# Kernel tuning notes

Hardware: AMD Instinct MI355X
Metric: run time of the kernel (lower is better)

The kernel has to match this reference:

```python
import jax, jax.numpy as jnp
import numpy as np

NOPE = 128          # qk_nope_head_dim
ROPE = 64           # qk_rope_head_dim
KV_LORA = 512       # kv_lora_rank
SCALE = (KV_LORA + ROPE) ** (-0.5)


def setup_inputs() -> dict:
    key = jax.random.key(0)
    k1, k2, k3, k4, k5 = jax.random.split(key, 5)
    T, H, K, S = 512, 128, 512, 8192
    q = jax.random.normal(k1, (T, H, NOPE + ROPE), dtype=jnp.float32)
    kv_cache = jax.random.normal(k2, (S, KV_LORA + ROPE), dtype=jnp.float32)
    topk_indices = jax.random.randint(k3, (T, K), 0, S, dtype=jnp.int32)
    k_b_proj_trans = jax.random.normal(k4, (H, KV_LORA, NOPE), dtype=jnp.float32) * 0.02
    v_b_proj = jax.random.normal(k5, (H, 128, KV_LORA), dtype=jnp.float32) * 0.02
    return {"q": q, "kv_cache": kv_cache, "topk_indices": topk_indices,
            "k_b_proj_trans": k_b_proj_trans, "v_b_proj": v_b_proj}


def reference(q, kv_cache, topk_indices, k_b_proj_trans, v_b_proj):
    # q: [T, H, 192]; kv_cache: [S, 576]; topk_indices: [T, K]
    q_nope, q_rope = q[..., :NOPE], q[..., NOPE:]
    # bmm_out(q_nope_t, k_b_proj_trans.transpose(1,2)): [T,H,128] x [H,512,128] -> [T,H,512]
    q_lat = jnp.einsum('thd,hkd->thk', q_nope, k_b_proj_trans)
    q_concat = jnp.concatenate([q_lat, q_rope], axis=-1)        # [T, H, 576]
    # sparse MLA: gather selected latent KV per token
    kv_sel = kv_cache[topk_indices]                              # [T, K, 576]
    scores = jnp.einsum('thc,tkc->thk', q_concat, kv_sel) * SCALE
    p = jax.nn.softmax(scores, axis=-1)                          # [T, H, K]
    attn_lat = jnp.einsum('thk,tkc->thc', p, kv_sel[..., :KV_LORA])  # [T, H, 512]
    # bmm_out(attn_lat_t, v_b_proj.transpose(1,2)): [T,H,512] x [H,512,128] -> [T,H,128]
    out = jnp.einsum('thc,hvc->thv', attn_lat, v_b_proj)
    return out
```

## Files before the change

### kernel.cpp

```cpp
#include <hip/hip_runtime.h>
#include <stdint.h>


#define SCALE 0.041666666666666664f

typedef __bf16 bf16x8 __attribute__((ext_vector_type(8)));
typedef float floatx4 __attribute__((ext_vector_type(4)));
typedef unsigned int uint32x2 __attribute__((ext_vector_type(2)));
typedef unsigned int uint32x4 __attribute__((ext_vector_type(4)));

static __device__ __forceinline__ unsigned short f2bf(float f) {
  unsigned int u = __builtin_bit_cast(unsigned int, f);
  u += 0x7FFF + ((u >> 16) & 1);
  return (unsigned short)(u >> 16);
}
static __device__ __forceinline__ float bf2f(unsigned short h) {
  unsigned int u = ((unsigned int)h) << 16;
  return __builtin_bit_cast(float, u);
}
static __device__ __forceinline__ unsigned int pack2(float lo, float hi) {
  return (unsigned int)f2bf(lo) | ((unsigned int)f2bf(hi) << 16);
}
static __device__ __forceinline__ void ldsdma16(const void* g, void* l) {
  __builtin_amdgcn_global_load_lds(
      (const __attribute__((address_space(1))) void*)g,
      (__attribute__((address_space(3))) void*)l, 16, 0, 0);
}
static __device__ __forceinline__ unsigned int lds_addr(const void* p) {
  return (unsigned int)(unsigned long long)(
      (__attribute__((address_space(3))) const void*)p);
}
#define TR64(dst, addr, OFF) \
  asm volatile("ds_read_b64_tr_b16 %0, %1 offset:" OFF : "=v"(dst) : "v"(addr))

static __device__ __forceinline__ void stage8_f32(const float* __restrict__ src,
                                                  unsigned short* dst) {
  const float4* s4 = reinterpret_cast<const float4*>(src);
  float4 v0 = s4[0], v1 = s4[1];
  uint4 o;
  o.x = pack2(v0.x, v0.y); o.y = pack2(v0.z, v0.w);
  o.z = pack2(v1.x, v1.y); o.w = pack2(v1.z, v1.w);
  *reinterpret_cast<uint4*>(dst) = o;
}

static __device__ __forceinline__ void mfma_4x4(const unsigned short* As,
                                                const unsigned short* Bs,
                                                int wm, int wn, int l15, int quad,
                                                floatx4 acc[4][4]) {
  bf16x8 af[4], bfr[4];
#pragma unroll
  for (int i = 0; i < 4; ++i)
    af[i] = *reinterpret_cast<const bf16x8*>(&As[(wm + i * 16 + l15) * 32 + quad * 8]);
#pragma unroll
  for (int j = 0; j < 4; ++j)
    bfr[j] = *reinterpret_cast<const bf16x8*>(&Bs[(wn + j * 16 + l15) * 32 + quad * 8]);
#pragma unroll
  for (int i = 0; i < 4; ++i)
#pragma unroll
    for (int j = 0; j < 4; ++j)
      acc[i][j] = __builtin_amdgcn_mfma_f32_16x16x32_bf16(af[i], bfr[j], acc[i][j], 0, 0, 0);
}

__global__ void prep(const float* __restrict__ kv, unsigned short* __restrict__ kvb,
                     const float* __restrict__ q, unsigned short* __restrict__ qc) {
  int b = blockIdx.x;
  if (b < 4608) {
    int i = b * 256 + threadIdx.x;
    float4 v = reinterpret_cast<const float4*>(kv)[i];
    ushort4 o;
    o.x = f2bf(v.x); o.y = f2bf(v.y); o.z = f2bf(v.z); o.w = f2bf(v.w);
    reinterpret_cast<ushort4*>(kvb)[i] = o;
  } else {
    int i = (b - 4608) * 256 + threadIdx.x;
    int r = i & 63;
    int th = i >> 6;
    qc[(size_t)th * 576 + 512 + r] = f2bf(q[(size_t)th * 192 + 128 + r] * SCALE);
  }
}

__global__ __launch_bounds__(256) void qlat_gemm(const float* __restrict__ q,
                                                 const float* __restrict__ kb,
                                                 unsigned short* __restrict__ qc) {
  const int h = blockIdx.x;
  const int tm = (blockIdx.y & 3) * 128;
  const int tn = (blockIdx.y >> 2) * 128;
  __shared__ __align__(16) unsigned short As[128 * 32];
  __shared__ __align__(16) unsigned short Bs[128 * 32];
  const int tid = threadIdx.x;
  const int lane = tid & 63, wave = tid >> 6;
  const int wm = (wave & 1) * 64, wn = (wave >> 1) * 64;
  const int l15 = lane & 15, quad = lane >> 4;
  const int r0 = tid >> 2, cg = tid & 3;
  const float* a0 = q + ((size_t)(tm + r0) * 128 + h) * 192 + cg * 8;
  const float* a1 = q + ((size_t)(tm + r0 + 64) * 128 + h) * 192 + cg * 8;
  const float* b0 = kb + ((size_t)h * 512 + tn + r0) * 128 + cg * 8;
  const float* b1 = b0 + (size_t)64 * 128;
  floatx4 acc[4][4] = {};
  for (int ks = 0; ks < 4; ++ks) {
    stage8_f32(a0 + ks * 32, &As[tid * 8]);
    stage8_f32(a1 + ks * 32, &As[2048 + tid * 8]);
    stage8_f32(b0 + ks * 32, &Bs[tid * 8]);
    stage8_f32(b1 + ks * 32, &Bs[2048 + tid * 8]);
    __syncthreads();
    mfma_4x4(As, Bs, wm, wn, l15, quad, acc);
    __syncthreads();
  }
#pragma unroll
  for (int i = 0; i < 4; ++i) {
    const int row = wm + i * 16 + quad * 4;
#pragma unroll
    for (int j = 0; j < 4; ++j) {
      const int col = wn + j * 16 + l15;
#pragma unroll
      for (int r = 0; r < 4; ++r) {
        const int t = tm + row + r;
        qc[((size_t)t * 128 + h) * 576 + tn + col] = f2bf(acc[i][j][r] * SCALE);
      }
    }
  }
}

__global__ __launch_bounds__(256) void scores_gemm(const unsigned short* __restrict__ qc,
                                                   const unsigned short* __restrict__ kvb,
                                                   const int* __restrict__ topk,
                                                   unsigned short* __restrict__ P) {
  const int t = blockIdx.x;
  const int tn = blockIdx.y * 128;
  __shared__ __align__(16) unsigned short As[3][128 * 32];
  __shared__ __align__(16) unsigned short Bs[3][128 * 32];
  const int tid = threadIdx.x;
  const int lane = tid & 63, wave = tid >> 6;
  const int wm = (wave & 1) * 64, wn = (wave >> 1) * 64;
  const int l15 = lane & 15, quad = lane >> 4;
  const int r0 = tid >> 2, cg = tid & 3;
  const unsigned short* a0 = qc + ((size_t)t * 128 + r0) * 576 + cg * 8;
  const unsigned short* a1 = a0 + (size_t)64 * 576;
  const int idx0 = topk[t * 512 + tn + r0];
  const int idx1 = topk[t * 512 + tn + r0 + 64];
  const unsigned short* b0 = kvb + (size_t)idx0 * 576 + cg * 8;
  const unsigned short* b1 = kvb + (size_t)idx1 * 576 + cg * 8;
  floatx4 acc[4][4] = {};
#pragma unroll
  for (int p = 0; p < 2; ++p) {
    ldsdma16(a0 + p * 32, &As[p][tid * 8]);
    ldsdma16(a1 + p * 32, &As[p][2048 + tid * 8]);
    ldsdma16(b0 + p * 32, &Bs[p][tid * 8]);
    ldsdma16(b1 + p * 32, &Bs[p][2048 + tid * 8]);
  }
  int bi = 0, bn = 2;
  for (int ks = 0; ks < 18; ++ks) {
    if (ks < 16) {
      ldsdma16(a0 + (ks + 2) * 32, &As[bn][tid * 8]);
      ldsdma16(a1 + (ks + 2) * 32, &As[bn][2048 + tid * 8]);
      ldsdma16(b0 + (ks + 2) * 32, &Bs[bn][tid * 8]);
      ldsdma16(b1 + (ks + 2) * 32, &Bs[bn][2048 + tid * 8]);
      asm volatile("s_waitcnt vmcnt(8)" ::: "memory");
    } else if (ks == 16) {
      asm volatile("s_waitcnt vmcnt(4)" ::: "memory");
    } else {
      asm volatile("s_waitcnt vmcnt(0)" ::: "memory");
    }
    __builtin_amdgcn_s_barrier();
    mfma_4x4(As[bi], Bs[bi], wm, wn, l15, quad, acc);
    __builtin_amdgcn_s_barrier();
    bi = bi == 2 ? 0 : bi + 1;
    bn = bn == 2 ? 0 : bn + 1;
  }
#pragma unroll
  for (int i = 0; i < 4; ++i) {
    const int row = wm + i * 16 + quad * 4;
#pragma unroll
    for (int j = 0; j < 4; ++j) {
      const int col = tn + wn + j * 16 + l15;
#pragma unroll
      for (int r = 0; r < 4; ++r)
        P[((size_t)t * 128 + row + r) * 512 + col] = f2bf(acc[i][j][r]);
    }
  }
}

__global__ __launch_bounds__(256) void softmax_rows(const unsigned short* __restrict__ Pin,
                                                    unsigned short* __restrict__ P2) {
  const int row = blockIdx.x * 4 + (threadIdx.x >> 6);
  const int t = row >> 7, h = row & 127;
  const int lane = threadIdx.x & 63;
  const unsigned short* rp = Pin + (size_t)row * 512 + lane * 8;
  uint4 raw = *reinterpret_cast<const uint4*>(rp);
  unsigned int w[4] = {raw.x, raw.y, raw.z, raw.w};
  float f[8];
  float mx = -1e30f;
#pragma unroll
  for (int i = 0; i < 8; ++i) {
    f[i] = bf2f((unsigned short)((w[i >> 1] >> ((i & 1) * 16)) & 0xFFFF));
    mx = fmaxf(mx, f[i]);
  }
#pragma unroll
  for (int off = 32; off; off >>= 1) mx = fmaxf(mx, __shfl_xor(mx, off, 64));
  float s = 0.f;
#pragma unroll
  for (int i = 0; i < 8; ++i) { f[i] = __expf(f[i] - mx); s += f[i]; }
#pragma unroll
  for (int off = 32; off; off >>= 1) s += __shfl_xor(s, off, 64);
  const float inv = 1.0f / s;
  uint4 o;
  o.x = pack2(f[0] * inv, f[1] * inv);
  o.y = pack2(f[2] * inv, f[3] * inv);
  o.z = pack2(f[4] * inv, f[5] * inv);
  o.w = pack2(f[6] * inv, f[7] * inv);
  unsigned short* wp =
      P2 + (((size_t)t * 16 + (lane >> 2)) * 128 + h) * 32 + (lane & 3) * 8;
  *reinterpret_cast<uint4*>(wp) = o;
}

__global__ __launch_bounds__(256) void attn_gemm(const unsigned short* __restrict__ P2,
                                                 const unsigned short* __restrict__ kvb,
                                                 const int* __restrict__ topk,
                                                 unsigned short* __restrict__ alat) {
  const int t = blockIdx.x;
  const int tn = blockIdx.y * 128;
  __shared__ __align__(16) unsigned short St[3][32 * 128];
  const int tid = threadIdx.x;
  const int lane = tid & 63, wave = tid >> 6;
  const int wm = (wave & 1) * 64, wn = (wave >> 1) * 64;
  const int l15 = lane & 15, quad = lane >> 4;
  const int keyA = wave * 4 + ((tid >> 1) & 3);
  const int cA = ((tid >> 3) & 7) * 16 + (tid & 1) * 8;
  const int* tkrow = topk + t * 512;
  const unsigned short* a_base =
      P2 + ((size_t)t * 16 * 128 + wm + l15) * 32 + quad * 8;
  const unsigned int tra0 = lds_addr(&St[0][0]) + quad * 2048 + wn * 8 + l15 * 8;
  floatx4 acc[4][4] = {};
  bf16x8 a_cur[4], a_nxt[4];
  int i0p, i1p;
  {
    const int i00 = tkrow[keyA], i10 = tkrow[16 + keyA];
    ldsdma16(kvb + (size_t)i00 * 576 + tn + cA, &St[0][tid * 8]);
    ldsdma16(kvb + (size_t)i10 * 576 + tn + cA, &St[0][2048 + tid * 8]);
    i0p = tkrow[64 + keyA];
    i1p = tkrow[80 + keyA];
#pragma unroll
    for (int i = 0; i < 4; ++i)
      a_cur[i] = *reinterpret_cast<const bf16x8*>(a_base + (size_t)i * 16 * 32);
    const int i01 = tkrow[32 + keyA], i11 = tkrow[48 + keyA];
    ldsdma16(kvb + (size_t)i01 * 576 + tn + cA, &St[1][tid * 8]);
    ldsdma16(kvb + (size_t)i11 * 576 + tn + cA, &St[1][2048 + tid * 8]);
  }
  int sti = 0, std2 = 2;
  for (int ks = 0; ks < 16; ++ks) {
    if (ks < 15) asm volatile("s_waitcnt vmcnt(2)" ::: "memory");
    else         asm volatile("s_waitcnt vmcnt(0)" ::: "memory");
    __builtin_amdgcn_s_barrier();
    const unsigned int tra = tra0 + sti * 8192;
    uint32x2 r00, r01, r10, r11, r20, r21, r30, r31;
    TR64(r00, tra, "0");   TR64(r01, tra, "1024");
    TR64(r10, tra, "128"); TR64(r11, tra, "1152");
    TR64(r20, tra, "256"); TR64(r21, tra, "1280");
    TR64(r30, tra, "384"); TR64(r31, tra, "1408");
    if (ks < 15) {
#pragma unroll
      for (int i = 0; i < 4; ++i)
        a_nxt[i] = *reinterpret_cast<const bf16x8*>(
            a_base + ((size_t)(ks + 1) * 128 + i * 16) * 32);
    }
    if (ks < 14) {
      const int d0 = i0p, d1 = i1p;
      if (ks < 13) {
        i0p = tkrow[(ks + 3) * 32 + keyA];
        i1p = tkrow[(ks + 3) * 32 + 16 + keyA];
      }
      ldsdma16(kvb + (size_t)d0 * 576 + tn + cA, &St[std2][tid * 8]);
      ldsdma16(kvb + (size_t)d1 * 576 + tn + cA, &St[std2][2048 + tid * 8]);
    }
    asm volatile("s_waitcnt lgkmcnt(0)");
    __builtin_amdgcn_sched_barrier(0);
    bf16x8 bfr[4];
    {
      uint32x4 w;
      w.x = r00.x; w.y = r00.y; w.z = r01.x; w.w = r01.y;
      bfr[0] = __builtin_bit_cast(bf16x8, w);
      w.x = r10.x; w.y = r10.y; w.z = r11.x; w.w = r11.y;
      bfr[1] = __builtin_bit_cast(bf16x8, w);
      w.x = r20.x; w.y = r20.y; w.z = r21.x; w.w = r21.y;
      bfr[2] = __builtin_bit_cast(bf16x8, w);
      w.x = r30.x; w.y = r30.y; w.z = r31.x; w.w = r31.y;
      bfr[3] = __builtin_bit_cast(bf16x8, w);
    }
#pragma unroll
    for (int i = 0; i < 4; ++i)
#pragma unroll
      for (int j = 0; j < 4; ++j)
        acc[i][j] =
            __builtin_amdgcn_mfma_f32_16x16x32_bf16(a_cur[i], bfr[j], acc[i][j], 0, 0, 0);
#pragma unroll
    for (int i = 0; i < 4; ++i) a_cur[i] = a_nxt[i];
    sti = sti == 2 ? 0 : sti + 1;
    std2 = std2 == 2 ? 0 : std2 + 1;
  }
#pragma unroll
  for (int i = 0; i < 4; ++i) {
    const int row = wm + i * 16 + quad * 4;
#pragma unroll
    for (int j = 0; j < 4; ++j) {
      const int col = tn + wn + j * 16 + l15;
#pragma unroll
      for (int r = 0; r < 4; ++r)
        alat[((size_t)(row + r) * 512 + t) * 512 + col] = f2bf(acc[i][j][r]);
    }
  }
}

__global__ __launch_bounds__(256) void out_gemm(const unsigned short* __restrict__ alat,
                                                const float* __restrict__ vb,
                                                float* __restrict__ out) {
  const int h = blockIdx.x;
  const int tm = blockIdx.y * 128;
  __shared__ __align__(16) unsigned short As[128 * 32];
  __shared__ __align__(16) unsigned short Bs[128 * 32];
  const int tid = threadIdx.x;
  const int lane = tid & 63, wave = tid >> 6;
  const int wm = (wave & 1) * 64, wn = (wave >> 1) * 64;
  const int l15 = lane & 15, quad = lane >> 4;
  const int r0 = tid >> 2, cg = tid & 3;
  const unsigned short* a0 = alat + ((size_t)h * 512 + tm + r0) * 512 + cg * 8;
  const unsigned short* a1 = a0 + (size_t)64 * 512;
  const float* b0 = vb + ((size_t)h * 128 + r0) * 512 + cg * 8;
  const float* b1 = b0 + (size_t)64 * 512;
  floatx4 acc[4][4] = {};
  for (int ks = 0; ks < 16; ++ks) {
    ldsdma16(a0 + ks * 32, &As[tid * 8]);
    ldsdma16(a1 + ks * 32, &As[2048 + tid * 8]);
    stage8_f32(b0 + ks * 32, &Bs[tid * 8]);
    stage8_f32(b1 + ks * 32, &Bs[2048 + tid * 8]);
    __syncthreads();
    mfma_4x4(As, Bs, wm, wn, l15, quad, acc);
    __syncthreads();
  }
#pragma unroll
  for (int i = 0; i < 4; ++i) {
    const int row = wm + i * 16 + quad * 4;
#pragma unroll
    for (int j = 0; j < 4; ++j) {
      const int col = wn + j * 16 + l15;
#pragma unroll
      for (int r = 0; r < 4; ++r) {
        const int t = tm + row + r;
        out[((size_t)t * 128 + h) * 128 + col] = acc[i][j][r];
      }
    }
  }
}

extern "C" void kernel_launch(void* const* d_in, const int* in_sizes, int n_in,
                              void* d_out, int out_size, void* d_ws, size_t ws_size,
                              hipStream_t stream) {
  const float* q = (const float*)d_in[0];
  const float* kv = (const float*)d_in[1];
  const int* topk = (const int*)d_in[2];
  const float* kb = (const float*)d_in[3];
  const float* vb = (const float*)d_in[4];
  float* out = (float*)d_out;

  char* ws = (char*)d_ws;
  unsigned short* kvb = (unsigned short*)ws;
  unsigned short* qc = (unsigned short*)(ws + 9437184);
  unsigned short* P = (unsigned short*)(ws + 9437184 + 75497472);
  unsigned short* P2 = qc;
  unsigned short* alat = P;

  prep<<<dim3(20992), dim3(256), 0, stream>>>(kv, kvb, q, qc);
  qlat_gemm<<<dim3(128, 16), dim3(256), 0, stream>>>(q, kb, qc);
  scores_gemm<<<dim3(512, 4), dim3(256), 0, stream>>>(qc, kvb, topk, P);
  softmax_rows<<<dim3(16384), dim3(256), 0, stream>>>(P, P2);
  attn_gemm<<<dim3(512, 4), dim3(256), 0, stream>>>(P2, kvb, topk, alat);
  out_gemm<<<dim3(128, 4), dim3(256), 0, stream>>>(alat, vb, out);
}
```

Before: 386.7 us.

## Widen attn_gemm to full 512-column tile per token and swap grid axes

attn_gemm now uses one 512-thread block per token covering all 512 latent columns, so each gathered KV row is loaded once per token rather than four times across column blocks, and the P tile is read once instead of four times. LDS staging grows to 3x32x512 bf16 and each wave holds a 4x8 accumulator tile, which raises register and LDS pressure and cuts the number of blocks to 512. The other GEMM launches swap grid x/y so neighbouring blocks share the same head or token, which is meant to improve L2 locality.

```diff
diff --git a/kernel.cpp b/kernel.cpp
--- a/kernel.cpp
+++ b/kernel.cpp
@@ -81,9 +81,9 @@
 __global__ __launch_bounds__(256) void qlat_gemm(const float* __restrict__ q,
                                                  const float* __restrict__ kb,
                                                  unsigned short* __restrict__ qc) {
-  const int h = blockIdx.x;
-  const int tm = (blockIdx.y & 3) * 128;
-  const int tn = (blockIdx.y >> 2) * 128;
+  const int h = blockIdx.y;
+  const int tm = (blockIdx.x & 3) * 128;
+  const int tn = (blockIdx.x >> 2) * 128;
   __shared__ __align__(16) unsigned short As[128 * 32];
   __shared__ __align__(16) unsigned short Bs[128 * 32];
   const int tid = threadIdx.x;
@@ -124,8 +124,8 @@
                                                    const unsigned short* __restrict__ kvb,
                                                    const int* __restrict__ topk,
                                                    unsigned short* __restrict__ P) {
-  const int t = blockIdx.x;
-  const int tn = blockIdx.y * 128;
+  const int t = blockIdx.y;
+  const int tn = blockIdx.x * 128;
   __shared__ __align__(16) unsigned short As[3][128 * 32];
   __shared__ __align__(16) unsigned short Bs[3][128 * 32];
   const int tid = threadIdx.x;
@@ -212,50 +212,60 @@
   *reinterpret_cast<uint4*>(wp) = o;
 }
 
-__global__ __launch_bounds__(256) void attn_gemm(const unsigned short* __restrict__ P2,
+__global__ __launch_bounds__(512) void attn_gemm(const unsigned short* __restrict__ P2,
                                                  const unsigned short* __restrict__ kvb,
                                                  const int* __restrict__ topk,
                                                  unsigned short* __restrict__ alat) {
   const int t = blockIdx.x;
-  const int tn = blockIdx.y * 128;
-  __shared__ __align__(16) unsigned short St[3][32 * 128];
+  __shared__ __align__(16) unsigned short St[3][32 * 512];
   const int tid = threadIdx.x;
   const int lane = tid & 63, wave = tid >> 6;
-  const int wm = (wave & 1) * 64, wn = (wave >> 1) * 64;
+  const int wm = (wave >> 2) * 64;
+  const int wc = wave & 3;
   const int l15 = lane & 15, quad = lane >> 4;
-  const int keyA = wave * 4 + ((tid >> 1) & 3);
-  const int cA = ((tid >> 3) & 7) * 16 + (tid & 1) * 8;
+  const int keyBase = (tid >> 8) * 4 + ((tid >> 1) & 3);
+  const int cA = ((tid >> 3) & 31) * 16 + (tid & 1) * 8;
   const int* tkrow = topk + t * 512;
   const unsigned short* a_base =
       P2 + ((size_t)t * 16 * 128 + wm + l15) * 32 + quad * 8;
-  const unsigned int tra0 = lds_addr(&St[0][0]) + quad * 2048 + wn * 8 + l15 * 8;
-  floatx4 acc[4][4] = {};
+  const unsigned int tra0 = lds_addr(&St[0][0]) + quad * 8192 + wc * 1024 + l15 * 8;
+  floatx4 acc[4][8] = {};
   bf16x8 a_cur[4], a_nxt[4];
-  int i0p, i1p;
+  int ip0, ip1, ip2, ip3;
   {
-    const int i00 = tkrow[keyA], i10 = tkrow[16 + keyA];
-    ldsdma16(kvb + (size_t)i00 * 576 + tn + cA, &St[0][tid * 8]);
-    ldsdma16(kvb + (size_t)i10 * 576 + tn + cA, &St[0][2048 + tid * 8]);
-    i0p = tkrow[64 + keyA];
-    i1p = tkrow[80 + keyA];
+#pragma unroll
+    for (int d = 0; d < 4; ++d) {
+      const int k0 = tkrow[d * 8 + keyBase];
+      ldsdma16(kvb + (size_t)k0 * 576 + cA, &St[0][d * 4096 + tid * 8]);
+    }
 #pragma unroll
     for (int i = 0; i < 4; ++i)
       a_cur[i] = *reinterpret_cast<const bf16x8*>(a_base + (size_t)i * 16 * 32);
-    const int i01 = tkrow[32 + keyA], i11 = tkrow[48 + keyA];
-    ldsdma16(kvb + (size_t)i01 * 576 + tn + cA, &St[1][tid * 8]);
-    ldsdma16(kvb + (size_t)i11 * 576 + tn + cA, &St[1][2048 + tid * 8]);
-  }
-  int sti = 0, std2 = 2;
+    ip0 = tkrow[64 + 0 * 8 + keyBase];
+    ip1 = tkrow[64 + 1 * 8 + keyBase];
+    ip2 = tkrow[64 + 2 * 8 + keyBase];
+    ip3 = tkrow[64 + 3 * 8 + keyBase];
+#pragma unroll
+    for (int d = 0; d < 4; ++d) {
+      const int k1 = tkrow[32 + d * 8 + keyBase];
+      ldsdma16(kvb + (size_t)k1 * 576 + cA, &St[1][d * 4096 + tid * 8]);
+    }
+  }
+  int sti = 0, stp = 2;
   for (int ks = 0; ks < 16; ++ks) {
-    if (ks < 15) asm volatile("s_waitcnt vmcnt(2)" ::: "memory");
-    else         asm volatile("s_waitcnt vmcnt(0)" ::: "memory");
+    asm volatile("s_waitcnt vmcnt(4)" ::: "memory");
     __builtin_amdgcn_s_barrier();
-    const unsigned int tra = tra0 + sti * 8192;
-    uint32x2 r00, r01, r10, r11, r20, r21, r30, r31;
-    TR64(r00, tra, "0");   TR64(r01, tra, "1024");
-    TR64(r10, tra, "128"); TR64(r11, tra, "1152");
-    TR64(r20, tra, "256"); TR64(r21, tra, "1280");
-    TR64(r30, tra, "384"); TR64(r31, tra, "1408");
+    const unsigned int tra = tra0 + sti * 32768;
+    uint32x2 rl0, rl1, rl2, rl3, rl4, rl5, rl6, rl7;
+    uint32x2 rh0, rh1, rh2, rh3, rh4, rh5, rh6, rh7;
+    TR64(rl0, tra, "0");    TR64(rh0, tra, "4096");
+    TR64(rl1, tra, "128");  TR64(rh1, tra, "4224");
+    TR64(rl2, tra, "256");  TR64(rh2, tra, "4352");
+    TR64(rl3, tra, "384");  TR64(rh3, tra, "4480");
+    TR64(rl4, tra, "512");  TR64(rh4, tra, "4608");
+    TR64(rl5, tra, "640");  TR64(rh5, tra, "4736");
+    TR64(rl6, tra, "768");  TR64(rh6, tra, "4864");
+    TR64(rl7, tra, "896");  TR64(rh7, tra, "4992");
     if (ks < 15) {
 #pragma unroll
       for (int i = 0; i < 4; ++i)
@@ -263,45 +273,49 @@
             a_base + ((size_t)(ks + 1) * 128 + i * 16) * 32);
     }
     if (ks < 14) {
-      const int d0 = i0p, d1 = i1p;
+      const int d0 = ip0, d1 = ip1, d2 = ip2, d3 = ip3;
       if (ks < 13) {
-        i0p = tkrow[(ks + 3) * 32 + keyA];
-        i1p = tkrow[(ks + 3) * 32 + 16 + keyA];
+        ip0 = tkrow[(ks + 3) * 32 + 0 * 8 + keyBase];
+        ip1 = tkrow[(ks + 3) * 32 + 1 * 8 + keyBase];
+        ip2 = tkrow[(ks + 3) * 32 + 2 * 8 + keyBase];
+        ip3 = tkrow[(ks + 3) * 32 + 3 * 8 + keyBase];
       }
-      ldsdma16(kvb + (size_t)d0 * 576 + tn + cA, &St[std2][tid * 8]);
-      ldsdma16(kvb + (size_t)d1 * 576 + tn + cA, &St[std2][2048 + tid * 8]);
+      ldsdma16(kvb + (size_t)d0 * 576 + cA, &St[stp][0 * 4096 + tid * 8]);
+      ldsdma16(kvb + (size_t)d1 * 576 + cA, &St[stp][1 * 4096 + tid * 8]);
+      ldsdma16(kvb + (size_t)d2 * 576 + cA, &St[stp][2 * 4096 + tid * 8]);
+      ldsdma16(kvb + (size_t)d3 * 576 + cA, &St[stp][3 * 4096 + tid * 8]);
     }
     asm volatile("s_waitcnt lgkmcnt(0)");
     __builtin_amdgcn_sched_barrier(0);
-    bf16x8 bfr[4];
+    bf16x8 bfr[8];
     {
       uint32x4 w;
-      w.x = r00.x; w.y = r00.y; w.z = r01.x; w.w = r01.y;
-      bfr[0] = __builtin_bit_cast(bf16x8, w);
-      w.x = r10.x; w.y = r10.y; w.z = r11.x; w.w = r11.y;
-      bfr[1] = __builtin_bit_cast(bf16x8, w);
-      w.x = r20.x; w.y = r20.y; w.z = r21.x; w.w = r21.y;
-      bfr[2] = __builtin_bit_cast(bf16x8, w);
-      w.x = r30.x; w.y = r30.y; w.z = r31.x; w.w = r31.y;
-      bfr[3] = __builtin_bit_cast(bf16x8, w);
+      w.x = rl0.x; w.y = rl0.y; w.z = rh0.x; w.w = rh0.y; bfr[0] = __builtin_bit_cast(bf16x8, w);
+      w.x = rl1.x; w.y = rl1.y; w.z = rh1.x; w.w = rh1.y; bfr[1] = __builtin_bit_cast(bf16x8, w);
+      w.x = rl2.x; w.y = rl2.y; w.z = rh2.x; w.w = rh2.y; bfr[2] = __builtin_bit_cast(bf16x8, w);
+      w.x = rl3.x; w.y = rl3.y; w.z = rh3.x; w.w = rh3.y; bfr[3] = __builtin_bit_cast(bf16x8, w);
+      w.x = rl4.x; w.y = rl4.y; w.z = rh4.x; w.w = rh4.y; bfr[4] = __builtin_bit_cast(bf16x8, w);
+      w.x = rl5.x; w.y = rl5.y; w.z = rh5.x; w.w = rh5.y; bfr[5] = __builtin_bit_cast(bf16x8, w);
+      w.x = rl6.x; w.y = rl6.y; w.z = rh6.x; w.w = rh6.y; bfr[6] = __builtin_bit_cast(bf16x8, w);
+      w.x = rl7.x; w.y = rl7.y; w.z = rh7.x; w.w = rh7.y; bfr[7] = __builtin_bit_cast(bf16x8, w);
     }
 #pragma unroll
     for (int i = 0; i < 4; ++i)
 #pragma unroll
-      for (int j = 0; j < 4; ++j)
+      for (int j = 0; j < 8; ++j)
         acc[i][j] =
             __builtin_amdgcn_mfma_f32_16x16x32_bf16(a_cur[i], bfr[j], acc[i][j], 0, 0, 0);
 #pragma unroll
     for (int i = 0; i < 4; ++i) a_cur[i] = a_nxt[i];
     sti = sti == 2 ? 0 : sti + 1;
-    std2 = std2 == 2 ? 0 : std2 + 1;
+    stp = stp == 2 ? 0 : stp + 1;
   }
 #pragma unroll
   for (int i = 0; i < 4; ++i) {
     const int row = wm + i * 16 + quad * 4;
 #pragma unroll
-    for (int j = 0; j < 4; ++j) {
-      const int col = tn + wn + j * 16 + l15;
+    for (int j = 0; j < 8; ++j) {
+      const int col = wc * 128 + j * 16 + l15;
 #pragma unroll
       for (int r = 0; r < 4; ++r)
         alat[((size_t)(row + r) * 512 + t) * 512 + col] = f2bf(acc[i][j][r]);
@@ -312,8 +326,8 @@
 __global__ __launch_bounds__(256) void out_gemm(const unsigned short* __restrict__ alat,
                                                 const float* __restrict__ vb,
                                                 float* __restrict__ out) {
-  const int h = blockIdx.x;
-  const int tm = blockIdx.y * 128;
+  const int h = blockIdx.y;
+  const int tm = blockIdx.x * 128;
   __shared__ __align__(16) unsigned short As[128 * 32];
   __shared__ __align__(16) unsigned short Bs[128 * 32];
   const int tid = threadIdx.x;
@@ -368,9 +382,9 @@
   unsigned short* alat = P;
 
   prep<<<dim3(20992), dim3(256), 0, stream>>>(kv, kvb, q, qc);
-  qlat_gemm<<<dim3(128, 16), dim3(256), 0, stream>>>(q, kb, qc);
-  scores_gemm<<<dim3(512, 4), dim3(256), 0, stream>>>(qc, kvb, topk, P);
+  qlat_gemm<<<dim3(16, 128), dim3(256), 0, stream>>>(q, kb, qc);
+  scores_gemm<<<dim3(4, 512), dim3(256), 0, stream>>>(qc, kvb, topk, P);
   softmax_rows<<<dim3(16384), dim3(256), 0, stream>>>(P, P2);
-  attn_gemm<<<dim3(512, 4), dim3(256), 0, stream>>>(P2, kvb, topk, alat);
-  out_gemm<<<dim3(128, 4), dim3(256), 0, stream>>>(alat, vb, out);
-}
+  attn_gemm<<<dim3(512), dim3(512), 0, stream>>>(P2, kvb, topk, alat);
+  out_gemm<<<dim3(4, 128), dim3(256), 0, stream>>>(alat, vb, out);
+}
```

New measurement: 383.9 us. No clear change (-0.7%).
